# Kernel tuning notes

Hardware: AMD Instinct MI355X
Metric: run time of the kernel (lower is better)

Reference implementation:

```python
import jax, jax.numpy as jnp
import numpy as np
from jax import lax

V, E, H, T, B = 32000, 512, 512, 64, 64

def _xavier(key, shape):
    fan_out, fan_in = shape
    std = np.sqrt(2.0 / (fan_in + fan_out))
    return jax.random.normal(key, shape, dtype=jnp.float32) * std

def setup_inputs() -> dict:
    key = jax.random.key(0)
    ks = jax.random.split(key, 12)
    scale = np.sqrt(3.0 / E)
    emb = jax.random.uniform(ks[0], (V, E), minval=-scale, maxval=scale, dtype=jnp.float32)
    return {
        "emb": emb,                                   # frozen embedding table [V,E]
        "W_ih": _xavier(ks[1], (3 * H, E)),           # GRU input weights (r,z,n stacked)
        "W_hh": _xavier(ks[2], (3 * H, H)),           # GRU hidden weights
        "b_ih": jnp.zeros((3 * H,), jnp.float32),
        "b_hh": jnp.zeros((3 * H,), jnp.float32),
        "zt_W": _xavier(ks[3], (H, E + H)), "zt_b": jnp.zeros((H,), jnp.float32),
        "rt_W": _xavier(ks[4], (E, E + H)), "rt_b": jnp.zeros((E,), jnp.float32),
        "ht_W": _xavier(ks[5], (H, E + H)), "ht_b": jnp.zeros((H,), jnp.float32),
        "dec_W": _xavier(ks[6], (V, H)), "dec_b": jnp.zeros((V,), jnp.float32),
        "init_hidden": jnp.zeros((1, B, H), jnp.float32),
        "word": jax.random.randint(ks[7], (B,), 0, V),
        "seq": jax.random.randint(ks[8], (T, B), 0, V),
    }

def reference(emb, W_ih, W_hh, b_ih, b_hh, zt_W, zt_b, rt_W, rt_b, ht_W, ht_b,
              dec_W, dec_b, init_hidden, word, seq):
    word_emb = emb[word]          # [B,E] (frozen)
    seq_emb = emb[seq]            # [T,B,E]
    h0 = init_hidden[0]           # [B,H], single layer

    def step(h, x):
        # standard torch GRU cell
        gi = x @ W_ih.T + b_ih    # [B,3H]
        gh = h @ W_hh.T + b_hh
        i_r, i_z, i_n = jnp.split(gi, 3, axis=-1)
        h_r, h_z, h_n = jnp.split(gh, 3, axis=-1)
        r = jax.nn.sigmoid(i_r + h_r)
        z = jax.nn.sigmoid(i_z + h_z)
        n = jnp.tanh(i_n + r * h_n)
        h_gru = (1.0 - z) * n + z * h      # rnn output at this step
        # extra GRU-style gating with word embedding (use_g branch)
        inp_h = jnp.concatenate([word_emb, h_gru], axis=-1)      # [B,E+H]
        zt = jax.nn.sigmoid(inp_h @ zt_W.T + zt_b)               # [B,H]
        rt = jax.nn.sigmoid(inp_h @ rt_W.T + rt_b)               # [B,E]
        hcat = jnp.concatenate([rt * word_emb, h_gru], axis=-1)  # [B,E+H]
        h_tilde = jnp.tanh(hcat @ ht_W.T + ht_b)                 # [B,H]
        h_new = (1.0 - zt) * h_gru + zt * h_tilde
        return h_new, h_gru

    h_final, outs = lax.scan(step, h0, seq_emb)   # outs [T,B,H]
    flat = outs.reshape(-1, H)                    # [T*B,H]
    decoded = flat @ dec_W.T + dec_b              # [T*B,V]
    return decoded, h_final[None]                 # hidden [1,B,H]
```

## Files before the change

kernel.cpp:

```cpp
#include <hip/hip_runtime.h>
#include <stdint.h>

#define GAS __attribute__((address_space(1)))
#define LAS __attribute__((address_space(3)))

typedef __bf16 bf16x8 __attribute__((ext_vector_type(8)));
typedef _Float16 f16x8 __attribute__((ext_vector_type(8)));
typedef float f32x4 __attribute__((ext_vector_type(4)));
typedef unsigned u32x4 __attribute__((ext_vector_type(4)));

__device__ __forceinline__ unsigned short f2bf(float f) {
  unsigned u = __float_as_uint(f);
  unsigned r = (u + 0x7FFFu + ((u >> 16) & 1u)) >> 16;
  return (unsigned short)r;
}

__device__ __forceinline__ float sigmoidf(float x) {
  return 1.f / (1.f + expf(-x));
}

__device__ __forceinline__ void st2c(_Float16* p, _Float16 v) {
  unsigned short u = __builtin_bit_cast(unsigned short, v);
  __hip_atomic_store((unsigned short*)p, u, __ATOMIC_RELAXED, __HIP_MEMORY_SCOPE_AGENT);
}
__device__ __forceinline__ void stu2c(unsigned short* p, unsigned short v) {
  __hip_atomic_store(p, v, __ATOMIC_RELAXED, __HIP_MEMORY_SCOPE_AGENT);
}
__device__ __forceinline__ void stf_mall(unsigned* p, unsigned v) {
  __hip_atomic_store(p, v, __ATOMIC_RELAXED, __HIP_MEMORY_SCOPE_AGENT);
}
__device__ __forceinline__ unsigned ldf_mall(const unsigned* p) {
  return __hip_atomic_load(p, __ATOMIC_RELAXED, __HIP_MEMORY_SCOPE_AGENT);
}
__device__ __forceinline__ u32x4 ld16_mall(const void* p) {
  u32x4 r;
  asm volatile("global_load_dwordx4 %0, %1, off sc0 sc1"
               : "=v"(r) : "v"(p) : "memory");
  return r;
}
template <int OFF>
__device__ __forceinline__ f16x8 ldh8_mall(const _Float16* p) {
  u32x4 r;
  asm volatile("global_load_dwordx4 %0, %1, off offset:%2 sc0 sc1"
               : "=v"(r) : "v"(p), "n"(OFF) : "memory");
  return __builtin_bit_cast(f16x8, r);
}

__global__ __launch_bounds__(128) void k_gather(
    const float* __restrict__ emb, const int* __restrict__ seq,
    const int* __restrict__ word, unsigned short* __restrict__ xbf,
    float* __restrict__ wemb) {
  int row = blockIdx.x;
  int tid = threadIdx.x;
  if (row < 4096) {
    const float* src = emb + (size_t)seq[row] * 512;
    unsigned short* dst = xbf + (size_t)row * 512;
    for (int e = tid; e < 512; e += 128) dst[e] = f2bf(src[e]);
  } else {
    int b = row - 4096;
    const float* src = emb + (size_t)word[b] * 512;
    float* dst = wemb + (size_t)b * 512;
    for (int e = tid; e < 512; e += 128) dst[e] = src[e];
  }
}

__global__ __launch_bounds__(128) void k_conv(
    const float* __restrict__ Wih, const float* __restrict__ decW,
    unsigned short* __restrict__ wih_bf, unsigned short* __restrict__ dec_bf) {
  int row = blockIdx.x;
  int tid = threadIdx.x;
  if (row < 1536) {
    const float* s = Wih + (size_t)row * 512;
    unsigned short* d = wih_bf + (size_t)row * 512;
    for (int e = tid; e < 512; e += 128) d[e] = f2bf(s[e]);
  } else {
    int o = row - 1536;
    const float* s = decW + (size_t)o * 512;
    unsigned short* d = dec_bf + (size_t)o * 512;
    for (int e = tid; e < 512; e += 128) d[e] = f2bf(s[e]);
  }
}

__global__ __launch_bounds__(256) void k_pre(
    const float* __restrict__ ztW, const float* __restrict__ ztb,
    const float* __restrict__ rtW, const float* __restrict__ rtb,
    const float* __restrict__ wemb, float* __restrict__ ztp,
    float* __restrict__ rtp) {
  int idx = blockIdx.x * 256 + threadIdx.x;
  int b = idx >> 10, o = idx & 1023;
  const float4* we = (const float4*)(wemb + (size_t)b * 512);
  const float4* wr;
  float acc;
  if (o < 512) { wr = (const float4*)(ztW + (size_t)o * 1024); acc = ztb[o]; }
  else { wr = (const float4*)(rtW + (size_t)(o - 512) * 1024); acc = rtb[o - 512]; }
  for (int c = 0; c < 128; ++c) {
    float4 w = wr[c], e = we[c];
    acc += w.x * e.x + w.y * e.y + w.z * e.z + w.w * e.w;
  }
  if (o < 512) ztp[(size_t)b * 512 + o] = acc;
  else rtp[(size_t)b * 512 + (o - 512)] = acc;
}

__global__ __launch_bounds__(256) void k_gemm_bt(
    const unsigned short* __restrict__ A, const unsigned short* __restrict__ B,
    float* __restrict__ C, const float* __restrict__ bias,
    int M, int N, int K) {
  __shared__ __align__(16) unsigned short As[128 * 32];
  __shared__ __align__(16) unsigned short Bs[128 * 32];
  int nt = N >> 7;
  int nwg = gridDim.x;
  int bid = blockIdx.x;
  int swz = (bid & 7) * (nwg >> 3) + (bid >> 3);
  int m0 = (swz / nt) << 7, n0 = (swz % nt) << 7;
  int tid = threadIdx.x;
  int l = tid & 63, w = tid >> 6;
  int wr = w >> 1, wc = w & 1;
  int lr = l & 15, lk = l >> 4;
  f32x4 acc[4][4] = {};
  for (int k0 = 0; k0 < K; k0 += 32) {
#pragma unroll
    for (int i = 0; i < 2; ++i) {
      int c = w * 2 + i;
      int off = c * 1024 + l * 16;
      int row = off >> 6, kb = off & 63;
      const char* ga = (const char*)A + ((size_t)(m0 + row) * K + k0) * 2 + kb;
      const char* gb = (const char*)B + ((size_t)(n0 + row) * K + k0) * 2 + kb;
      __builtin_amdgcn_global_load_lds((const GAS void*)ga,
                                       (LAS void*)((char*)As + c * 1024), 16, 0, 0);
      __builtin_amdgcn_global_load_lds((const GAS void*)gb,
                                       (LAS void*)((char*)Bs + c * 1024), 16, 0, 0);
    }
    asm volatile("s_waitcnt vmcnt(0)" ::: "memory");
    __syncthreads();
    bf16x8 af[4], bfr[4];
#pragma unroll
    for (int i = 0; i < 4; ++i)
      af[i] = *(const bf16x8*)&As[(wr * 64 + i * 16 + lr) * 32 + lk * 8];
#pragma unroll
    for (int i = 0; i < 4; ++i)
      bfr[i] = *(const bf16x8*)&Bs[(wc * 64 + i * 16 + lr) * 32 + lk * 8];
#pragma unroll
    for (int i = 0; i < 4; ++i)
#pragma unroll
      for (int jj = 0; jj < 4; ++jj)
        acc[i][jj] = __builtin_amdgcn_mfma_f32_16x16x32_bf16(af[i], bfr[jj], acc[i][jj], 0, 0, 0);
    __syncthreads();
  }
#pragma unroll
  for (int jj = 0; jj < 4; ++jj) {
    int col = n0 + wc * 64 + jj * 16 + lr;
    float bv = bias ? bias[col] : 0.f;
#pragma unroll
    for (int i = 0; i < 4; ++i) {
      int rb = m0 + wr * 64 + i * 16 + lk * 4;
#pragma unroll
      for (int q = 0; q < 4; ++q)
        C[(size_t)(rb + q) * N + col] = acc[i][jj][q] + bv;
    }
  }
}

struct MegaP {
  const float *Whh, *ztW, *rtW, *htW;
  const float *gi, *ztp, *rtp, *wemb, *inith, *bhh, *htb;
  _Float16 *hcurF, *hgruF, *rwF;
  unsigned short *outsb;
  float *hfin;
  unsigned *flags;
  const unsigned short *decbf;
  const float *decb;
  float *outC;
};

__device__ __forceinline__ void poll_band(const unsigned* flags, int w, int l,
                                          unsigned tgt) {
  const unsigned* fp = flags + ((size_t)((l & 31) * 4 + w)) * 16;
  for (;;) {
    unsigned v = ldf_mall(fp);
    if (__all((int)(v >= tgt))) break;
  }
}

template <int NT>
__device__ __forceinline__ void mm_mall(f32x4* acc, const _Float16* A,
                                        const _Float16* WLrow, int w, int lr, int lk) {
  f16x8 af[16];
  const _Float16* arow = A + ((size_t)(16 * w + lr)) * 512 + lk * 8;
#define LDA(c) af[c] = ldh8_mall<(c) * 64>(arow);
  LDA(0) LDA(1) LDA(2) LDA(3) LDA(4) LDA(5) LDA(6) LDA(7)
  LDA(8) LDA(9) LDA(10) LDA(11) LDA(12) LDA(13) LDA(14) LDA(15)
#undef LDA
  asm volatile("s_waitcnt vmcnt(0)" ::: "memory");
  __builtin_amdgcn_sched_barrier(0);
#pragma unroll
  for (int c = 0; c < 16; ++c) {
#pragma unroll
    for (int n = 0; n < NT; ++n) {
      f16x8 bb = *(const f16x8*)(WLrow + (n * 16 + lr) * 520 + c * 32 + lk * 8);
      acc[n] = __builtin_amdgcn_mfma_f32_16x16x32_f16(af[c], bb, acc[n], 0, 0, 0);
    }
  }
}

__global__ __launch_bounds__(256) void k_mega(MegaP p) {
  __shared__ __align__(16) char LSD[116480];
  const int tid = threadIdx.x;
  const int w = tid >> 6, l = tid & 63;
  const int lr = l & 15, lk = l >> 4;

  if (blockIdx.x < 32) {
    const int g = blockIdx.x;
    _Float16* WL = (_Float16*)LSD;
    for (int idx = tid; idx < 112 * 512; idx += 256) {
      int rr = idx >> 9, e = idx & 511;
      const float* src;
      if (rr < 48) {
        int gate = rr >> 4, i = rr & 15;
        src = p.Whh + ((size_t)(gate * 512 + g * 16 + i)) * 512 + e;
      } else if (rr < 96) {
        int r2 = rr - 48, gate = r2 >> 4, i = r2 & 15;
        const float* base = gate == 0 ? p.ztW : (gate == 1 ? p.rtW : p.htW);
        src = base + ((size_t)(g * 16 + i)) * 1024 + 512 + e;
      } else {
        int i = rr - 96;
        src = p.htW + ((size_t)(g * 16 + i)) * 1024 + e;
      }
      WL[rr * 520 + e] = (_Float16)(*src);
    }
    const int j = g * 16 + lr;
    const int brow = 16 * w + lk * 4;
    f32x4 hprev, zp, rp, wev;
#pragma unroll
    for (int q = 0; q < 4; ++q) {
      int b = brow + q;
      hprev[q] = p.inith[(size_t)b * 512 + j];
      zp[q] = p.ztp[(size_t)b * 512 + j];
      rp[q] = p.rtp[(size_t)b * 512 + j];
      wev[q] = p.wemb[(size_t)b * 512 + j];
      st2c(&p.hcurF[(size_t)b * 512 + j], (_Float16)hprev[q]);
    }
    const float br = p.bhh[j], bz = p.bhh[512 + j], bn = p.bhh[1024 + j];
    const float bht = p.htb[j];
    float gir[12];
#pragma unroll
    for (int q = 0; q < 4; ++q) {
      const float* git = p.gi + (size_t)(brow + q) * 1536;
      gir[q * 3 + 0] = git[j];
      gir[q * 3 + 1] = git[512 + j];
      gir[q * 3 + 2] = git[1024 + j];
    }
    __syncthreads();
    asm volatile("s_waitcnt vmcnt(0)" ::: "memory");
    if (tid == 0) stf_mall(p.flags + (size_t)(g * 4 + 0) * 16, 1u);
    else if (tid == 64) stf_mall(p.flags + (size_t)(g * 4 + 1) * 16, 1u);
    else if (tid == 128) stf_mall(p.flags + (size_t)(g * 4 + 2) * 16, 1u);
    else if (tid == 192) stf_mall(p.flags + (size_t)(g * 4 + 3) * 16, 1u);

    for (int t = 0; t < 64; ++t) {
      const unsigned base = 3u * (unsigned)t;
      poll_band(p.flags, w, l, base + 1);
      f32x4 acc1[3] = {};
      mm_mall<3>(acc1, p.hcurF, &WL[0], w, lr, lk);
      f32x4 hg;
#pragma unroll
      for (int q = 0; q < 4; ++q) {
        int b = brow + q;
        float r = sigmoidf(gir[q * 3 + 0] + br + acc1[0][q]);
        float z = sigmoidf(gir[q * 3 + 1] + bz + acc1[1][q]);
        float n = tanhf(gir[q * 3 + 2] + r * (acc1[2][q] + bn));
        float hgq = (1.f - z) * n + z * hprev[q];
        hg[q] = hgq;
        st2c(&p.hgruF[(size_t)b * 512 + j], (_Float16)hgq);
        stu2c(&p.outsb[((size_t)t * 64 + b) * 512 + j], f2bf(hgq));
      }
      asm volatile("s_waitcnt vmcnt(0)" ::: "memory");
      if (l == 0) stf_mall(p.flags + ((size_t)(g * 4 + w)) * 16, base + 2);
      poll_band(p.flags, w, l, base + 2);
      f32x4 acc2[3] = {};
      mm_mall<3>(acc2, p.hgruF, &WL[48 * 520], w, lr, lk);
      f32x4 zt, htB;
#pragma unroll
      for (int q = 0; q < 4; ++q) {
        int b = brow + q;
        float ztq = sigmoidf(zp[q] + acc2[0][q]);
        float rtq = sigmoidf(rp[q] + acc2[1][q]);
        zt[q] = ztq;
        htB[q] = acc2[2][q];
        st2c(&p.rwF[(size_t)b * 512 + j], (_Float16)(rtq * wev[q]));
      }
      asm volatile("s_waitcnt vmcnt(0)" ::: "memory");
      if (l == 0) stf_mall(p.flags + ((size_t)(g * 4 + w)) * 16, base + 3);
      if (t < 63) {
        const float* git = p.gi + (size_t)(t + 1) * 64 * 1536;
#pragma unroll
        for (int q = 0; q < 4; ++q) {
          const float* gb = git + (size_t)(brow + q) * 1536;
          gir[q * 3 + 0] = gb[j];
          gir[q * 3 + 1] = gb[512 + j];
          gir[q * 3 + 2] = gb[1024 + j];
        }
      }
      poll_band(p.flags, w, l, base + 3);
      f32x4 acc3[1] = {};
      mm_mall<1>(acc3, p.rwF, &WL[96 * 520], w, lr, lk);
#pragma unroll
      for (int q = 0; q < 4; ++q) {
        int b = brow + q;
        float htl = tanhf(acc3[0][q] + htB[q] + bht);
        float hn2 = (1.f - zt[q]) * hg[q] + zt[q] * htl;
        hprev[q] = hn2;
        if (t < 63) st2c(&p.hcurF[(size_t)b * 512 + j], (_Float16)hn2);
        else p.hfin[(size_t)b * 512 + j] = hn2;
      }
      if (t < 63) {
        asm volatile("s_waitcnt vmcnt(0)" ::: "memory");
        if (l == 0) stf_mall(p.flags + ((size_t)(g * 4 + w)) * 16, base + 4);
      }
    }
  } else {
    const int d = blockIdx.x - 32;
    unsigned short* As = (unsigned short*)LSD;
    unsigned short* Bs = (unsigned short*)(LSD + 64 * 520 * 2);
    for (int t = 0; t < 64; ++t) {
      const unsigned tgt = 3u * (unsigned)t + 2u;
      {
        const unsigned* f0 = p.flags + (size_t)l * 16;
        const unsigned* f1 = p.flags + (size_t)(l + 64) * 16;
        for (;;) {
          unsigned a = ldf_mall(f0);
          unsigned b = ldf_mall(f1);
          if (__all((int)(a >= tgt && b >= tgt))) break;
        }
      }
      __syncthreads();
      {
        u32x4 av[8];
#pragma unroll
        for (int it = 0; it < 8; ++it) {
          int fi = (tid + 256 * it) * 8;
          av[it] = ld16_mall(p.outsb + ((size_t)t * 64 + (fi >> 9)) * 512 + (fi & 511));
        }
        asm volatile("s_waitcnt vmcnt(0)" ::: "memory");
#pragma unroll
        for (int it = 0; it < 8; ++it) {
          int fi = (tid + 256 * it) * 8;
          *(u32x4*)&As[(fi >> 9) * 520 + (fi & 511)] = av[it];
        }
#pragma unroll
        for (int it = 8; it < 16; ++it) {
          int fi = (tid + 256 * it) * 8;
          av[it - 8] = ld16_mall(p.outsb + ((size_t)t * 64 + (fi >> 9)) * 512 + (fi & 511));
        }
        asm volatile("s_waitcnt vmcnt(0)" ::: "memory");
#pragma unroll
        for (int it = 8; it < 16; ++it) {
          int fi = (tid + 256 * it) * 8;
          *(u32x4*)&As[(fi >> 9) * 520 + (fi & 511)] = av[it - 8];
        }
      }
      __syncthreads();
#pragma unroll 1
      for (int tix = 0; tix < 2; ++tix) {
        int tile = d + tix * 224;
        if (tile >= 250) break;
        int n0 = tile * 128;
        f32x4 acc[8] = {};
        for (int k0 = 0; k0 < 512; k0 += 32) {
#pragma unroll
          for (int i = 0; i < 2; ++i) {
            int c = w * 2 + i;
            int off = c * 1024 + l * 16;
            int row = off >> 6, kb = off & 63;
            const char* gb = (const char*)p.decbf + ((size_t)(n0 + row) * 512 + k0) * 2 + kb;
            __builtin_amdgcn_global_load_lds((const GAS void*)gb,
                                             (LAS void*)((char*)Bs + c * 1024), 16, 0, 0);
          }
          asm volatile("s_waitcnt vmcnt(0)" ::: "memory");
          __syncthreads();
          bf16x8 af = *(const bf16x8*)&As[(16 * w + lr) * 520 + k0 + lk * 8];
#pragma unroll
          for (int n = 0; n < 8; ++n) {
            bf16x8 bfr = *(const bf16x8*)&Bs[(n * 16 + lr) * 32 + lk * 8];
            acc[n] = __builtin_amdgcn_mfma_f32_16x16x32_bf16(af, bfr, acc[n], 0, 0, 0);
          }
          __syncthreads();
        }
#pragma unroll
        for (int n = 0; n < 8; ++n) {
          int col = n0 + n * 16 + lr;
          float bv = p.decb[col];
#pragma unroll
          for (int q = 0; q < 4; ++q) {
            int row = t * 64 + 16 * w + lk * 4 + q;
            p.outC[(size_t)row * 32000 + col] = acc[n][q] + bv;
          }
        }
      }
    }
  }
}

extern "C" void kernel_launch(void* const* d_in, const int* in_sizes, int n_in,
                              void* d_out, int out_size, void* d_ws, size_t ws_size,
                              hipStream_t stream) {
  const float* emb   = (const float*)d_in[0];
  const float* Wih   = (const float*)d_in[1];
  const float* Whh   = (const float*)d_in[2];
  const float* bih   = (const float*)d_in[3];
  const float* bhh   = (const float*)d_in[4];
  const float* ztW   = (const float*)d_in[5];
  const float* ztb   = (const float*)d_in[6];
  const float* rtW   = (const float*)d_in[7];
  const float* rtb   = (const float*)d_in[8];
  const float* htW   = (const float*)d_in[9];
  const float* htb   = (const float*)d_in[10];
  const float* decW  = (const float*)d_in[11];
  const float* decb  = (const float*)d_in[12];
  const float* inith = (const float*)d_in[13];
  const int* word    = (const int*)d_in[14];
  const int* seq     = (const int*)d_in[15];
  float* out = (float*)d_out;

  char* ws = (char*)d_ws;
  size_t off = 0;
  auto alloc = [&](size_t bytes) {
    size_t o = off;
    off += (bytes + 255) & ~(size_t)255;
    return o;
  };
  unsigned short* xbf   = (unsigned short*)(ws + alloc(4096ull * 512 * 2));
  unsigned short* wihbf = (unsigned short*)(ws + alloc(1536ull * 512 * 2));
  unsigned short* decbf = (unsigned short*)(ws + alloc(32000ull * 512 * 2));
  float* wemb           = (float*)(ws + alloc(64ull * 512 * 4));
  float* ztp            = (float*)(ws + alloc(64ull * 512 * 4));
  float* rtp            = (float*)(ws + alloc(64ull * 512 * 4));
  float* gi             = (float*)(ws + alloc(4096ull * 1536 * 4));
  unsigned short* outsb = (unsigned short*)(ws + alloc(4096ull * 512 * 2));
  _Float16* hcurF       = (_Float16*)(ws + alloc(64ull * 512 * 2));
  _Float16* hgruF       = (_Float16*)(ws + alloc(64ull * 512 * 2));
  _Float16* rwF         = (_Float16*)(ws + alloc(64ull * 512 * 2));
  unsigned* flags       = (unsigned*)(ws + alloc(128 * 64));

  hipLaunchKernelGGL(k_gather, dim3(4160), dim3(128), 0, stream,
                     emb, seq, word, xbf, wemb);
  hipLaunchKernelGGL(k_conv, dim3(33536), dim3(128), 0, stream,
                     Wih, decW, wihbf, decbf);
  hipLaunchKernelGGL(k_pre, dim3(256), dim3(256), 0, stream,
                     ztW, ztb, rtW, rtb, wemb, ztp, rtp);
  hipLaunchKernelGGL(k_gemm_bt, dim3(384), dim3(256), 0, stream,
                     xbf, wihbf, gi, bih, 4096, 1536, 512);
  hipMemsetAsync(flags, 0, 128 * 64, stream);
  MegaP p{Whh, ztW, rtW, htW, gi, ztp, rtp, wemb, inith, bhh, htb,
          hcurF, hgruF, rwF, outsb, out + 4096ull * 32000, flags,
          decbf, decb, out};
  hipLaunchKernelGGL(k_mega, dim3(256), dim3(256), 0, stream, p);
}
```

Before: 1.429 ms.

## Move outs store and gi prefetch off the recurrence critical path; DMA outs to LDS

In the recurrent blocks, the bf16 outs store moves after the step-2 flag is published, and the next step's gi prefetch is hoisted earlier so both overlap the wait on other blocks. The decoder blocks now wait for flag base+3 instead of base+2, because outs is written after the base+2 flag. They load the outs row tile straight into LDS with global_load_lds instead of going through registers, and back off with s_sleep while polling. The aim is a shorter serial GRU step and less polling traffic competing with the recurrence. In exchange the decoder starts each timestep slightly later, and the direct load relies on the flag ordering to see fresh data.

```diff
diff --git a/kernel.cpp b/kernel.cpp
--- a/kernel.cpp
+++ b/kernel.cpp
@@ -31,12 +31,6 @@
 }
 __device__ __forceinline__ unsigned ldf_mall(const unsigned* p) {
   return __hip_atomic_load(p, __ATOMIC_RELAXED, __HIP_MEMORY_SCOPE_AGENT);
-}
-__device__ __forceinline__ u32x4 ld16_mall(const void* p) {
-  u32x4 r;
-  asm volatile("global_load_dwordx4 %0, %1, off sc0 sc1"
-               : "=v"(r) : "v"(p) : "memory");
-  return r;
 }
 template <int OFF>
 __device__ __forceinline__ f16x8 ldh8_mall(const _Float16* p) {
@@ -160,7 +154,7 @@
   }
 }
 
-struct MegaP {
+struct FusedP {
   const float *Whh, *ztW, *rtW, *htW;
   const float *gi, *ztp, *rtp, *wemb, *inith, *bhh, *htb;
   _Float16 *hcurF, *hgruF, *rwF;
@@ -202,7 +196,7 @@
   }
 }
 
-__global__ __launch_bounds__(256) void k_mega(MegaP p) {
+__global__ __launch_bounds__(256) void k_fused(FusedP p) {
   __shared__ __align__(16) char LSD[116480];
   const int tid = threadIdx.x;
   const int w = tid >> 6, l = tid & 63;
@@ -210,6 +204,7 @@
 
   if (blockIdx.x < 32) {
     const int g = blockIdx.x;
+    unsigned* myflag = p.flags + ((size_t)(g * 4 + w)) * 16;
     _Float16* WL = (_Float16*)LSD;
     for (int idx = tid; idx < 112 * 512; idx += 256) {
       int rr = idx >> 9, e = idx & 511;
@@ -250,11 +245,7 @@
       gir[q * 3 + 2] = git[1024 + j];
     }
     __syncthreads();
-    asm volatile("s_waitcnt vmcnt(0)" ::: "memory");
-    if (tid == 0) stf_mall(p.flags + (size_t)(g * 4 + 0) * 16, 1u);
-    else if (tid == 64) stf_mall(p.flags + (size_t)(g * 4 + 1) * 16, 1u);
-    else if (tid == 128) stf_mall(p.flags + (size_t)(g * 4 + 2) * 16, 1u);
-    else if (tid == 192) stf_mall(p.flags + (size_t)(g * 4 + 3) * 16, 1u);
+    if (l == 0) stf_mall(myflag, 1u);
 
     for (int t = 0; t < 64; ++t) {
       const unsigned base = 3u * (unsigned)t;
@@ -271,10 +262,22 @@
         float hgq = (1.f - z) * n + z * hprev[q];
         hg[q] = hgq;
         st2c(&p.hgruF[(size_t)b * 512 + j], (_Float16)hgq);
-        stu2c(&p.outsb[((size_t)t * 64 + b) * 512 + j], f2bf(hgq));
       }
       asm volatile("s_waitcnt vmcnt(0)" ::: "memory");
-      if (l == 0) stf_mall(p.flags + ((size_t)(g * 4 + w)) * 16, base + 2);
+      if (l == 0) stf_mall(myflag, base + 2);
+#pragma unroll
+      for (int q = 0; q < 4; ++q)
+        stu2c(&p.outsb[((size_t)t * 64 + brow + q) * 512 + j], f2bf(hg[q]));
+      if (t < 63) {
+        const float* git = p.gi + (size_t)(t + 1) * 64 * 1536;
+#pragma unroll
+        for (int q = 0; q < 4; ++q) {
+          const float* gb = git + (size_t)(brow + q) * 1536;
+          gir[q * 3 + 0] = gb[j];
+          gir[q * 3 + 1] = gb[512 + j];
+          gir[q * 3 + 2] = gb[1024 + j];
+        }
+      }
       poll_band(p.flags, w, l, base + 2);
       f32x4 acc2[3] = {};
       mm_mall<3>(acc2, p.hgruF, &WL[48 * 520], w, lr, lk);
@@ -289,17 +292,7 @@
         st2c(&p.rwF[(size_t)b * 512 + j], (_Float16)(rtq * wev[q]));
       }
       asm volatile("s_waitcnt vmcnt(0)" ::: "memory");
-      if (l == 0) stf_mall(p.flags + ((size_t)(g * 4 + w)) * 16, base + 3);
-      if (t < 63) {
-        const float* git = p.gi + (size_t)(t + 1) * 64 * 1536;
-#pragma unroll
-        for (int q = 0; q < 4; ++q) {
-          const float* gb = git + (size_t)(brow + q) * 1536;
-          gir[q * 3 + 0] = gb[j];
-          gir[q * 3 + 1] = gb[512 + j];
-          gir[q * 3 + 2] = gb[1024 + j];
-        }
-      }
+      if (l == 0) stf_mall(myflag, base + 3);
       poll_band(p.flags, w, l, base + 3);
       f32x4 acc3[1] = {};
       mm_mall<1>(acc3, p.rwF, &WL[96 * 520], w, lr, lk);
@@ -314,7 +307,7 @@
       }
       if (t < 63) {
         asm volatile("s_waitcnt vmcnt(0)" ::: "memory");
-        if (l == 0) stf_mall(p.flags + ((size_t)(g * 4 + w)) * 16, base + 4);
+        if (l == 0) stf_mall(myflag, base + 4);
       }
     }
   } else {
@@ -322,7 +315,7 @@
     unsigned short* As = (unsigned short*)LSD;
     unsigned short* Bs = (unsigned short*)(LSD + 64 * 520 * 2);
     for (int t = 0; t < 64; ++t) {
-      const unsigned tgt = 3u * (unsigned)t + 2u;
+      const unsigned tgt = 3u * (unsigned)t + 3u;
       {
         const unsigned* f0 = p.flags + (size_t)l * 16;
         const unsigned* f1 = p.flags + (size_t)(l + 64) * 16;
@@ -330,34 +323,18 @@
           unsigned a = ldf_mall(f0);
           unsigned b = ldf_mall(f1);
           if (__all((int)(a >= tgt && b >= tgt))) break;
+          __builtin_amdgcn_s_sleep(8);
         }
       }
-      __syncthreads();
-      {
-        u32x4 av[8];
-#pragma unroll
-        for (int it = 0; it < 8; ++it) {
-          int fi = (tid + 256 * it) * 8;
-          av[it] = ld16_mall(p.outsb + ((size_t)t * 64 + (fi >> 9)) * 512 + (fi & 511));
-        }
-        asm volatile("s_waitcnt vmcnt(0)" ::: "memory");
-#pragma unroll
-        for (int it = 0; it < 8; ++it) {
-          int fi = (tid + 256 * it) * 8;
-          *(u32x4*)&As[(fi >> 9) * 520 + (fi & 511)] = av[it];
-        }
-#pragma unroll
-        for (int it = 8; it < 16; ++it) {
-          int fi = (tid + 256 * it) * 8;
-          av[it - 8] = ld16_mall(p.outsb + ((size_t)t * 64 + (fi >> 9)) * 512 + (fi & 511));
-        }
-        asm volatile("s_waitcnt vmcnt(0)" ::: "memory");
-#pragma unroll
-        for (int it = 8; it < 16; ++it) {
-          int fi = (tid + 256 * it) * 8;
-          *(u32x4*)&As[(fi >> 9) * 520 + (fi & 511)] = av[it - 8];
-        }
-      }
+      for (int r = 0; r < 16; ++r) {
+        int row = w * 16 + r;
+        const char* src =
+            (const char*)(p.outsb + ((size_t)t * 64 + row) * 512) + l * 16;
+        __builtin_amdgcn_global_load_lds((const GAS void*)src,
+                                         (LAS void*)((char*)As + row * 1040),
+                                         16, 0, 0);
+      }
+      asm volatile("s_waitcnt vmcnt(0)" ::: "memory");
       __syncthreads();
 #pragma unroll 1
       for (int tix = 0; tix < 2; ++tix) {
@@ -371,9 +348,11 @@
             int c = w * 2 + i;
             int off = c * 1024 + l * 16;
             int row = off >> 6, kb = off & 63;
-            const char* gb = (const char*)p.decbf + ((size_t)(n0 + row) * 512 + k0) * 2 + kb;
+            const char* gb =
+                (const char*)p.decbf + ((size_t)(n0 + row) * 512 + k0) * 2 + kb;
             __builtin_amdgcn_global_load_lds((const GAS void*)gb,
-                                             (LAS void*)((char*)Bs + c * 1024), 16, 0, 0);
+                                             (LAS void*)((char*)Bs + c * 1024),
+                                             16, 0, 0);
           }
           asm volatile("s_waitcnt vmcnt(0)" ::: "memory");
           __syncthreads();
@@ -450,8 +429,8 @@
   hipLaunchKernelGGL(k_gemm_bt, dim3(384), dim3(256), 0, stream,
                      xbf, wihbf, gi, bih, 4096, 1536, 512);
   hipMemsetAsync(flags, 0, 128 * 64, stream);
-  MegaP p{Whh, ztW, rtW, htW, gi, ztp, rtp, wemb, inith, bhh, htb,
-          hcurF, hgruF, rwF, outsb, out + 4096ull * 32000, flags,
-          decbf, decb, out};
-  hipLaunchKernelGGL(k_mega, dim3(256), dim3(256), 0, stream, p);
-}
+  FusedP p{Whh, ztW, rtW, htW, gi, ztp, rtp, wemb, inith, bhh, htb,
+           hcurF, hgruF, rwF, outsb, out + 4096ull * 32000, flags,
+           decbf, decb, out};
+  hipLaunchKernelGGL(k_fused, dim3(256), dim3(256), 0, stream, p);
+}
```

Measured after the change: 1.375 ms. 1.04x faster.
